# Kernel optimization log

Measured on AMD Instinct MI355X. Metric: run time of the kernel, lower is better.

Reference implementation:

```python
import jax, jax.numpy as jnp
import numpy as np

B, S, D = 4, 2048, 768

def setup_inputs() -> dict:
    key = jax.random.key(0)
    ks = jax.random.split(key, 7)
    scale = 1.0 / np.sqrt(D)
    x = jax.random.normal(ks[0], (B, S, D), dtype=jnp.float32)
    Wq = jax.random.uniform(ks[1], (D, D), jnp.float32, -scale, scale)
    bq = jax.random.uniform(ks[2], (D,), jnp.float32, -scale, scale)
    Wk = jax.random.uniform(ks[3], (D, D), jnp.float32, -scale, scale)
    bk = jax.random.uniform(ks[4], (D,), jnp.float32, -scale, scale)
    Wv = jax.random.uniform(ks[5], (D, D), jnp.float32, -scale, scale)
    bv = jax.random.uniform(ks[6], (D,), jnp.float32, -scale, scale)
    return {"x": x, "Wq": Wq, "bq": bq, "Wk": Wk, "bk": bk, "Wv": Wv, "bv": bv}

def reference(x, Wq, bq, Wk, bk, Wv, bv):
    d = x.shape[-1]
    q = jnp.einsum('bsd,de->bse', x, Wq) + bq
    k = jnp.einsum('bsd,de->bse', x, Wk) + bk
    v = jnp.einsum('bsd,de->bse', x, Wv) + bv
    scores = jnp.einsum('bqd,bkd->bqk', q, k) / jnp.sqrt(jnp.asarray(d, x.dtype))
    attn = jax.nn.softmax(scores, axis=-1)  # [B,S,S]
    return jnp.einsum('bqk,bkd->bqd', attn, v)
```

## Files before the change

### kernel.cpp

```cpp
#include <hip/hip_runtime.h>
#include <hip/hip_bf16.h>


typedef __attribute__((ext_vector_type(8))) short short8;
typedef __attribute__((ext_vector_type(4))) short short4v;
typedef __attribute__((ext_vector_type(4))) float float4v;

static constexpr int B_ = 4, S_ = 2048, D_ = 768;
static constexpr int MS = B_ * S_;

__device__ inline short f2bf(float f) {
  __hip_bfloat16 h = __float2bfloat16(f);
  union { __hip_bfloat16 h; short s; } u; u.h = h; return u.s;
}

typedef const __attribute__((address_space(1))) unsigned int g_u32;
typedef __attribute__((address_space(3))) unsigned int l_u32;

__device__ __forceinline__ void glds16(const short* g, short* l) {
  __builtin_amdgcn_global_load_lds((g_u32*)g, (l_u32*)l, 16, 0, 0);
}

__global__ __launch_bounds__(256)
void cast_f32_bf16(const float* __restrict__ x, short* __restrict__ y, int n) {
  int i = (blockIdx.x * 256 + threadIdx.x) * 4;
  if (i + 3 < n) {
    float4v v = *(const float4v*)(x + i);
    short4v o;
    o.x = f2bf(v.x); o.y = f2bf(v.y); o.z = f2bf(v.z); o.w = f2bf(v.w);
    *(short4v*)(y + i) = o;
  }
}

__global__ void transpose_cast_w(const float* __restrict__ W0, const float* __restrict__ W1,
                                 const float* __restrict__ W2,
                                 short* __restrict__ T0, short* __restrict__ T1,
                                 short* __restrict__ T2) {
  const float* W = blockIdx.z == 0 ? W0 : (blockIdx.z == 1 ? W1 : W2);
  short* T = blockIdx.z == 0 ? T0 : (blockIdx.z == 1 ? T1 : T2);
  __shared__ float tile[32][33];
  int bx = blockIdx.x * 32, by = blockIdx.y * 32;
  int tx = threadIdx.x, ty = threadIdx.y;
  for (int r = ty; r < 32; r += 8)
    tile[r][tx] = W[(by + r) * D_ + bx + tx];
  __syncthreads();
  for (int r = ty; r < 32; r += 8)
    T[(bx + r) * D_ + by + tx] = f2bf(tile[tx][r]);
}

template<int EPI, int TM, int TN>
__global__ __launch_bounds__(256)
void gemm_bt(const short* __restrict__ A, const short* __restrict__ Bt,
             void* __restrict__ C0v, short* __restrict__ C1, short* __restrict__ C2,
             const float* __restrict__ bias0, const float* __restrict__ bias1,
             const float* __restrict__ bias2,
             int K, int lda, int ldb, int ldc,
             long sA, long sB, long sC, float scale) {
  constexpr int BMv = TM * 32, BNv = TN * 32;
  const int b = blockIdx.z;
  A += (long)b * sA;
  Bt += (long)b * sB;
  float* Cf = (float*)C0v + (long)b * sC;
  short* Cs = (short*)C0v + (long)b * sC;

  __shared__ short As[BMv * 64];
  __shared__ short Bs[BNv * 64];

  const int t = threadIdx.x;
  const int wave = t >> 6, lane = t & 63;
  const int lane16 = lane & 15, q = lane >> 4;
  const int m0 = blockIdx.y * BMv, n0 = blockIdx.x * BNv;
  const int wm = (wave >> 1) * (TM * 16), wn = (wave & 1) * (TN * 16);
  const int rsub = lane >> 3;
  const int g = (lane & 7) ^ rsub;

  auto stage = [&](int kk) {
#pragma unroll
    for (int i = wave; i < BMv / 8; i += 4)
      glds16(A + (long)(m0 + i * 8 + rsub) * lda + kk + g * 8, &As[i * 512]);
#pragma unroll
    for (int i = wave; i < BNv / 8; i += 4)
      glds16(Bt + (long)(n0 + i * 8 + rsub) * ldb + kk + g * 8, &Bs[i * 512]);
  };

  stage(0);

  float4v acc[TM][TN];
#pragma unroll
  for (int i = 0; i < TM; i++)
#pragma unroll
    for (int j = 0; j < TN; j++) acc[i][j] = {0.f, 0.f, 0.f, 0.f};

  float4v acc_rs[TM];
#pragma unroll
  for (int i = 0; i < TM; i++) acc_rs[i] = {0.f, 0.f, 0.f, 0.f};
  short8 ones;
#pragma unroll
  for (int e = 0; e < 8; e++) ones[e] = (short)0x3F80;

  for (int k0 = 0; k0 < K; k0 += 64) {
    __syncthreads();

    short8 af[2][TM], bfr[2][TN];
#pragma unroll
    for (int s = 0; s < 2; s++) {
#pragma unroll
      for (int i = 0; i < TM; i++) {
        int R = wm + i * 16 + lane16;
        af[s][i] = *(const short8*)&As[R * 64 + (((s * 4 + q) ^ (R & 7)) * 8)];
      }
#pragma unroll
      for (int j = 0; j < TN; j++) {
        int R = wn + j * 16 + lane16;
        bfr[s][j] = *(const short8*)&Bs[R * 64 + (((s * 4 + q) ^ (R & 7)) * 8)];
      }
    }
    __syncthreads();

    if (k0 + 64 < K) stage(k0 + 64);

#pragma unroll
    for (int s = 0; s < 2; s++) {
#pragma unroll
      for (int i = 0; i < TM; i++) {
#pragma unroll
        for (int j = 0; j < TN; j++)
          acc[i][j] = __builtin_amdgcn_mfma_f32_16x16x32_bf16(af[s][i], bfr[s][j], acc[i][j], 0, 0, 0);
        if (EPI == 3)
          acc_rs[i] = __builtin_amdgcn_mfma_f32_16x16x32_bf16(af[s][i], ones, acc_rs[i], 0, 0, 0);
      }
    }
  }

#pragma unroll
  for (int i = 0; i < TM; i++) {
    int mrow = m0 + wm + i * 16 + q * 4;
    if (EPI == 0) {
#pragma unroll
      for (int j = 0; j < TN; j++) {
        int ncol = n0 + wn + j * 16 + lane16;
        if (ncol < 1536) {
          short* dst = ncol < 768 ? Cs : C1;
          const float* bs = ncol < 768 ? bias0 : bias1;
          int c = ncol < 768 ? ncol : ncol - 768;
#pragma unroll
          for (int rr = 0; rr < 4; rr++)
            dst[(long)(mrow + rr) * 768 + c] = f2bf(acc[i][j][rr] + bs[c]);
        } else {
          int e = ncol - 1536;
          float bv = bias2[e];
          short4v o;
#pragma unroll
          for (int rr = 0; rr < 4; rr++) o[rr] = f2bf(acc[i][j][rr] + bv);
          *(short4v*)&C2[(long)e * MS + mrow] = o;
        }
      }
    } else if (EPI == 2) {
#pragma unroll
      for (int j = 0; j < TN; j++) {
        int ncol = n0 + wn + j * 16 + lane16;
#pragma unroll
        for (int rr = 0; rr < 4; rr++)
          Cs[(long)(mrow + rr) * ldc + ncol] = f2bf(__expf(acc[i][j][rr] * scale));
      }
    } else {
#pragma unroll
      for (int rr = 0; rr < 4; rr++) {
        float inv = 1.0f / acc_rs[i][rr];
#pragma unroll
        for (int j = 0; j < TN; j++) {
          int ncol = n0 + wn + j * 16 + lane16;
          Cf[(long)(mrow + rr) * ldc + ncol] = acc[i][j][rr] * inv;
        }
      }
    }
  }
}

template<int EPI>
__global__ __launch_bounds__(512, 2)
void gemm8p(const short* __restrict__ A, const short* __restrict__ Bt,
            void* __restrict__ C0v, short* __restrict__ C1, short* __restrict__ C2,
            const float* __restrict__ bias0, const float* __restrict__ bias1,
            const float* __restrict__ bias2,
            int K, int lda, int ldb, int ldc,
            long sA, long sB, long sC, float scale) {
  const int b = blockIdx.z;
  A += (long)b * sA;
  Bt += (long)b * sB;
  short* Cs = (short*)C0v + (long)b * sC;

  __shared__ short As[2][256 * 64];
  __shared__ short Bs[2][256 * 64];

  const int t = threadIdx.x;
  const int wave = t >> 6, lane = t & 63;
  const int lane16 = lane & 15, q = lane >> 4;
  const int xr = lane16 & 7;
  const int m0 = blockIdx.y * 256, n0 = blockIdx.x * 256;
  const int wm = (wave >> 2) * 128, wn = (wave & 3) * 64;
  const int rsub = lane >> 3;
  const int g = (lane & 7) ^ rsub;
  const int nt = K >> 6;

  auto stageA = [&](int u, int tt) {
    short* dst = &As[tt & 1][0];
    const short* src = A + tt * 64 + g * 8;
#pragma unroll
    for (int r = 0; r < 2; r++) {
      int row0 = u * 64 + r * 128 + wave * 8;
      glds16(src + (long)(m0 + row0 + rsub) * lda, dst + row0 * 64);
    }
  };
  auto stageB = [&](int u, int tt) {
    short* dst = &Bs[tt & 1][0];
    const short* src = Bt + tt * 64 + g * 8;
#pragma unroll
    for (int r = 0; r < 2; r++) {
      int idx = r * 8 + wave;
      int row0 = (idx >> 2) * 64 + u * 32 + (idx & 3) * 8;
      glds16(src + (long)(n0 + row0 + rsub) * ldb, dst + row0 * 64);
    }
  };

  float4v acc[8][4];
#pragma unroll
  for (int i = 0; i < 8; i++)
#pragma unroll
    for (int j = 0; j < 4; j++) acc[i][j] = {0.f, 0.f, 0.f, 0.f};

  stageA(0, 0); stageA(1, 0); stageB(0, 0); stageB(1, 0);
  if (nt > 1) { stageA(0, 1); stageB(0, 1); stageA(1, 1); }
  if (nt > 1) asm volatile("s_waitcnt vmcnt(6)" ::: "memory");
  else        asm volatile("s_waitcnt vmcnt(0)" ::: "memory");
  __builtin_amdgcn_s_barrier();

#pragma unroll 2
  for (int tt = 0; tt < nt; ++tt) {
    const short* Ab = &As[tt & 1][0];
    const short* Bb = &Bs[tt & 1][0];
    short8 a[4][2], b0[2][2], b1[2][2];

#pragma unroll
    for (int ii = 0; ii < 4; ii++) {
      int R = wm + ii * 16 + lane16;
#pragma unroll
      for (int s = 0; s < 2; s++)
        a[ii][s] = *(const short8*)&Ab[R * 64 + (((s * 4 + q) ^ xr) * 8)];
    }
#pragma unroll
    for (int jj = 0; jj < 2; jj++) {
      int R = wn + jj * 16 + lane16;
#pragma unroll
      for (int s = 0; s < 2; s++)
        b0[jj][s] = *(const short8*)&Bb[R * 64 + (((s * 4 + q) ^ xr) * 8)];
    }
    if (tt + 1 < nt) stageB(1, tt + 1);
    __builtin_amdgcn_s_barrier();
    asm volatile("s_waitcnt lgkmcnt(0)" ::: "memory");
    __builtin_amdgcn_sched_barrier(0);
    __builtin_amdgcn_s_setprio(1);
#pragma unroll
    for (int s = 0; s < 2; s++)
#pragma unroll
      for (int ii = 0; ii < 4; ii++)
#pragma unroll
        for (int jj = 0; jj < 2; jj++)
          acc[ii][jj] = __builtin_amdgcn_mfma_f32_16x16x32_bf16(a[ii][s], b0[jj][s], acc[ii][jj], 0, 0, 0);
    __builtin_amdgcn_s_setprio(0);
    __builtin_amdgcn_s_barrier();

#pragma unroll
    for (int jj = 0; jj < 2; jj++) {
      int R = wn + 32 + jj * 16 + lane16;
#pragma unroll
      for (int s = 0; s < 2; s++)
        b1[jj][s] = *(const short8*)&Bb[R * 64 + (((s * 4 + q) ^ xr) * 8)];
    }
    if (tt + 2 < nt) stageA(0, tt + 2);
    __builtin_amdgcn_s_barrier();
    asm volatile("s_waitcnt lgkmcnt(0)" ::: "memory");
    __builtin_amdgcn_sched_barrier(0);
    __builtin_amdgcn_s_setprio(1);
#pragma unroll
    for (int s = 0; s < 2; s++)
#pragma unroll
      for (int ii = 0; ii < 4; ii++)
#pragma unroll
        for (int jj = 0; jj < 2; jj++)
          acc[ii][2 + jj] = __builtin_amdgcn_mfma_f32_16x16x32_bf16(a[ii][s], b1[jj][s], acc[ii][2 + jj], 0, 0, 0);
    __builtin_amdgcn_s_setprio(0);
    __builtin_amdgcn_s_barrier();

#pragma unroll
    for (int ii = 0; ii < 4; ii++) {
      int R = wm + 64 + ii * 16 + lane16;
#pragma unroll
      for (int s = 0; s < 2; s++)
        a[ii][s] = *(const short8*)&Ab[R * 64 + (((s * 4 + q) ^ xr) * 8)];
    }
    if (tt + 2 < nt) stageB(0, tt + 2);
    __builtin_amdgcn_s_barrier();
    asm volatile("s_waitcnt lgkmcnt(0)" ::: "memory");
    __builtin_amdgcn_sched_barrier(0);
    __builtin_amdgcn_s_setprio(1);
#pragma unroll
    for (int s = 0; s < 2; s++)
#pragma unroll
      for (int ii = 0; ii < 4; ii++)
#pragma unroll
        for (int jj = 0; jj < 2; jj++)
          acc[4 + ii][2 + jj] = __builtin_amdgcn_mfma_f32_16x16x32_bf16(a[ii][s], b1[jj][s], acc[4 + ii][2 + jj], 0, 0, 0);
    __builtin_amdgcn_s_setprio(0);
    __builtin_amdgcn_s_barrier();

    if (tt + 2 < nt) stageA(1, tt + 2);
    __builtin_amdgcn_s_barrier();
    __builtin_amdgcn_s_setprio(1);
#pragma unroll
    for (int s = 0; s < 2; s++)
#pragma unroll
      for (int ii = 0; ii < 4; ii++)
#pragma unroll
        for (int jj = 0; jj < 2; jj++)
          acc[4 + ii][jj] = __builtin_amdgcn_mfma_f32_16x16x32_bf16(a[ii][s], b0[jj][s], acc[4 + ii][jj], 0, 0, 0);
    __builtin_amdgcn_s_setprio(0);
    if (tt + 2 < nt) asm volatile("s_waitcnt vmcnt(6)" ::: "memory");
    else             asm volatile("s_waitcnt vmcnt(0)" ::: "memory");
    __builtin_amdgcn_s_barrier();
  }

#pragma unroll
  for (int i = 0; i < 8; i++) {
    int mrow = m0 + wm + i * 16 + q * 4;
    if (EPI == 0) {
#pragma unroll
      for (int j = 0; j < 4; j++) {
        int ncol = n0 + wn + j * 16 + lane16;
        if (ncol < 1536) {
          short* dst = ncol < 768 ? Cs : C1;
          const float* bs = ncol < 768 ? bias0 : bias1;
          int c = ncol < 768 ? ncol : ncol - 768;
#pragma unroll
          for (int rr = 0; rr < 4; rr++)
            dst[(long)(mrow + rr) * 768 + c] = f2bf(acc[i][j][rr] + bs[c]);
        } else {
          int e = ncol - 1536;
          float bv = bias2[e];
          short4v o;
#pragma unroll
          for (int rr = 0; rr < 4; rr++) o[rr] = f2bf(acc[i][j][rr] + bv);
          *(short4v*)&C2[(long)e * MS + mrow] = o;
        }
      }
    } else {
#pragma unroll
      for (int j = 0; j < 4; j++) {
        int ncol = n0 + wn + j * 16 + lane16;
#pragma unroll
        for (int rr = 0; rr < 4; rr++)
          Cs[(long)(mrow + rr) * ldc + ncol] = f2bf(__expf(acc[i][j][rr] * scale));
      }
    }
  }
}

extern "C" void kernel_launch(void* const* d_in, const int* in_sizes, int n_in,
                              void* d_out, int out_size, void* d_ws, size_t ws_size,
                              hipStream_t stream) {
  const float* x  = (const float*)d_in[0];
  const float* Wq = (const float*)d_in[1];
  const float* bq = (const float*)d_in[2];
  const float* Wk = (const float*)d_in[3];
  const float* bk = (const float*)d_in[4];
  const float* Wv = (const float*)d_in[5];
  const float* bv = (const float*)d_in[6];
  float* out = (float*)d_out;

  short* Xb  = (short*)d_ws;
  short* WqT = Xb + (long)MS * D_;
  short* WkT = WqT + (long)D_ * D_;
  short* WvT = WkT + (long)D_ * D_;
  short* Qb  = WvT + (long)D_ * D_;
  short* Kb  = Qb + (long)MS * D_;
  short* Vt  = Kb + (long)MS * D_;
  short* Es  = Vt + (long)MS * D_;

  cast_f32_bf16<<<(MS * D_) / 1024, 256, 0, stream>>>(x, Xb, MS * D_);
  transpose_cast_w<<<dim3(24, 24, 3), dim3(32, 8), 0, stream>>>(Wq, Wk, Wv, WqT, WkT, WvT);

  gemm8p<0><<<dim3(2304 / 256, MS / 256, 1), 512, 0, stream>>>(
      Xb, WqT, Qb, Kb, Vt, bq, bk, bv,
      D_, D_, D_, D_, 0, 0, 0, 1.0f);
  gemm8p<2><<<dim3(S_ / 256, S_ / 256, B_), 512, 0, stream>>>(
      Qb, Kb, Es, nullptr, nullptr, nullptr, nullptr, nullptr,
      D_, D_, D_, S_,
      (long)S_ * D_, (long)S_ * D_, (long)S_ * S_, 1.0f / sqrtf((float)D_));
  gemm_bt<3, 4, 4><<<dim3(D_ / 128, S_ / 128, B_), 256, 0, stream>>>(
      Es, Vt, out, nullptr, nullptr, nullptr, nullptr, nullptr,
      S_, S_, MS, D_,
      (long)S_ * S_, (long)S_, (long)S_ * D_, 1.0f);
}
```

Measured before the change: 222.2 us.

## Swap PV GEMM operands so V is the M side and move QKV projection to gemm_bt

The final attention-times-V GEMM now puts Vt on the A side and the exp-score matrix on the B side. The row-sum normalisation is computed per column tile with a ones-vector MFMA, and the output is written transposed as float4 stores. The QKV projection launch moves from the 256-tile gemm8p kernel to the 128-tile gemm_bt kernel, and gemm8p's bias epilogue is removed. The intent is to cut redundant row-sum MFMAs and get vectorised output stores, at the cost of a different tile and occupancy profile for the projection GEMM.

Result: faster. 196.5 us (-11.5%).

```diff
diff --git a/kernel.cpp b/kernel.cpp
--- a/kernel.cpp
+++ b/kernel.cpp
@@ -91,9 +91,10 @@
 #pragma unroll
     for (int j = 0; j < TN; j++) acc[i][j] = {0.f, 0.f, 0.f, 0.f};
 
-  float4v acc_rs[TM];
-#pragma unroll
-  for (int i = 0; i < TM; i++) acc_rs[i] = {0.f, 0.f, 0.f, 0.f};
+  constexpr int NRS = TM > TN ? TM : TN;
+  float4v acc_rs[NRS];
+#pragma unroll
+  for (int i = 0; i < NRS; i++) acc_rs[i] = {0.f, 0.f, 0.f, 0.f};
   short8 ones;
 #pragma unroll
   for (int e = 0; e < 8; e++) ones[e] = (short)0x3F80;
@@ -121,13 +122,16 @@
 
 #pragma unroll
     for (int s = 0; s < 2; s++) {
+      if (EPI == 4) {
+#pragma unroll
+        for (int j = 0; j < TN; j++)
+          acc_rs[j] = __builtin_amdgcn_mfma_f32_16x16x32_bf16(ones, bfr[s][j], acc_rs[j], 0, 0, 0);
+      }
 #pragma unroll
       for (int i = 0; i < TM; i++) {
 #pragma unroll
         for (int j = 0; j < TN; j++)
           acc[i][j] = __builtin_amdgcn_mfma_f32_16x16x32_bf16(af[s][i], bfr[s][j], acc[i][j], 0, 0, 0);
-        if (EPI == 3)
-          acc_rs[i] = __builtin_amdgcn_mfma_f32_16x16x32_bf16(af[s][i], ones, acc_rs[i], 0, 0, 0);
       }
     }
   }
@@ -155,23 +159,15 @@
           *(short4v*)&C2[(long)e * MS + mrow] = o;
         }
       }
-    } else if (EPI == 2) {
+    } else {
 #pragma unroll
       for (int j = 0; j < TN; j++) {
         int ncol = n0 + wn + j * 16 + lane16;
-#pragma unroll
-        for (int rr = 0; rr < 4; rr++)
-          Cs[(long)(mrow + rr) * ldc + ncol] = f2bf(__expf(acc[i][j][rr] * scale));
-      }
-    } else {
-#pragma unroll
-      for (int rr = 0; rr < 4; rr++) {
-        float inv = 1.0f / acc_rs[i][rr];
-#pragma unroll
-        for (int j = 0; j < TN; j++) {
-          int ncol = n0 + wn + j * 16 + lane16;
-          Cf[(long)(mrow + rr) * ldc + ncol] = acc[i][j][rr] * inv;
-        }
+        float inv = 1.0f / acc_rs[j][0];
+        float4v o;
+#pragma unroll
+        for (int rr = 0; rr < 4; rr++) o[rr] = acc[i][j][rr] * inv;
+        *(float4v*)&Cf[(long)ncol * ldc + mrow] = o;
       }
     }
   }
@@ -333,34 +329,12 @@
 #pragma unroll
   for (int i = 0; i < 8; i++) {
     int mrow = m0 + wm + i * 16 + q * 4;
-    if (EPI == 0) {
-#pragma unroll
-      for (int j = 0; j < 4; j++) {
-        int ncol = n0 + wn + j * 16 + lane16;
-        if (ncol < 1536) {
-          short* dst = ncol < 768 ? Cs : C1;
-          const float* bs = ncol < 768 ? bias0 : bias1;
-          int c = ncol < 768 ? ncol : ncol - 768;
-#pragma unroll
-          for (int rr = 0; rr < 4; rr++)
-            dst[(long)(mrow + rr) * 768 + c] = f2bf(acc[i][j][rr] + bs[c]);
-        } else {
-          int e = ncol - 1536;
-          float bv = bias2[e];
-          short4v o;
-#pragma unroll
-          for (int rr = 0; rr < 4; rr++) o[rr] = f2bf(acc[i][j][rr] + bv);
-          *(short4v*)&C2[(long)e * MS + mrow] = o;
-        }
-      }
-    } else {
-#pragma unroll
-      for (int j = 0; j < 4; j++) {
-        int ncol = n0 + wn + j * 16 + lane16;
-#pragma unroll
-        for (int rr = 0; rr < 4; rr++)
-          Cs[(long)(mrow + rr) * ldc + ncol] = f2bf(__expf(acc[i][j][rr] * scale));
-      }
+#pragma unroll
+    for (int j = 0; j < 4; j++) {
+      int ncol = n0 + wn + j * 16 + lane16;
+#pragma unroll
+      for (int rr = 0; rr < 4; rr++)
+        Cs[(long)(mrow + rr) * ldc + ncol] = f2bf(__expf(acc[i][j][rr] * scale));
     }
   }
 }
@@ -389,15 +363,15 @@
   cast_f32_bf16<<<(MS * D_) / 1024, 256, 0, stream>>>(x, Xb, MS * D_);
   transpose_cast_w<<<dim3(24, 24, 3), dim3(32, 8), 0, stream>>>(Wq, Wk, Wv, WqT, WkT, WvT);
 
-  gemm8p<0><<<dim3(2304 / 256, MS / 256, 1), 512, 0, stream>>>(
+  gemm_bt<0, 4, 4><<<dim3(2304 / 128, MS / 128, 1), 256, 0, stream>>>(
       Xb, WqT, Qb, Kb, Vt, bq, bk, bv,
       D_, D_, D_, D_, 0, 0, 0, 1.0f);
   gemm8p<2><<<dim3(S_ / 256, S_ / 256, B_), 512, 0, stream>>>(
       Qb, Kb, Es, nullptr, nullptr, nullptr, nullptr, nullptr,
       D_, D_, D_, S_,
       (long)S_ * D_, (long)S_ * D_, (long)S_ * S_, 1.0f / sqrtf((float)D_));
-  gemm_bt<3, 4, 4><<<dim3(D_ / 128, S_ / 128, B_), 256, 0, stream>>>(
-      Es, Vt, out, nullptr, nullptr, nullptr, nullptr, nullptr,
-      S_, S_, MS, D_,
-      (long)S_ * S_, (long)S_, (long)S_ * D_, 1.0f);
-}
+  gemm_bt<4, 4, 4><<<dim3(S_ / 128, D_ / 128, B_), 256, 0, stream>>>(
+      Vt, Es, out, nullptr, nullptr, nullptr, nullptr, nullptr,
+      S_, MS, S_, D_,
+      (long)S_, (long)S_ * S_, (long)S_ * D_, 1.0f);
+}
```
